# Kernel tuning notes

Measured on AMD Instinct MI355X. Metric: run time of the kernel, lower is better.

Reference implementation:

```python
import jax, jax.numpy as jnp
import numpy as np

N = 12288
E = N * 32  # avg degree 32


def spmm(row, col, w, support):
    # out[i] = sum_{e: row[e]==i} w[e] * support[col[e]]
    return jax.ops.segment_sum(w[:, None] * support[col], row, num_segments=N)


def setup_inputs() -> dict:
    key = jax.random.key(0)
    ks = jax.random.split(key, 7)
    x = jax.random.normal(ks[0], (N, 512), dtype=jnp.float32)
    edge_row = jax.random.randint(ks[1], (E,), 0, N, dtype=jnp.int32)
    edge_col = jax.random.randint(ks[2], (E,), 0, N, dtype=jnp.int32)
    # row-normalized-ish positive edge weights
    edge_w = jax.random.uniform(ks[3], (E,), dtype=jnp.float32) / 32.0
    def xavier(k, fan_in, fan_out):
        bound = float(np.sqrt(6.0 / (fan_in + fan_out)))
        return jax.random.uniform(k, (fan_in, fan_out), jnp.float32, -bound, bound)
    W1 = xavier(ks[4], 512, 256)
    W2 = xavier(ks[5], 256, 128)
    W3 = xavier(ks[6], 128, 64)
    return {"x": x, "edge_row": edge_row, "edge_col": edge_col,
            "edge_w": edge_w, "W1": W1, "W2": W2, "W3": W3}


def reference(x, edge_row, edge_col, edge_w, W1, W2, W3):
    # GNNLayer 1 (active=True): tanh(x @ W) then spmm(adj, .)
    z1 = spmm(edge_row, edge_col, edge_w, jnp.tanh(x @ W1))
    # GNNLayer 2 (active=True)
    z2 = spmm(edge_row, edge_col, edge_w, jnp.tanh(z1 @ W2))
    # GNNLayer 3 (active=False): no activation
    z_igae = spmm(edge_row, edge_col, edge_w, z2 @ W3)  # [N, 64]
    # reconstructed adjacency: sigmoid(z z^T), [N, N]
    z_igae_adj = jax.nn.sigmoid(z_igae @ z_igae.T)
    return (z_igae, z_igae_adj)
```

## Files before the change

kernel.cpp:

```cpp
#include <hip/hip_runtime.h>
#include <hip/hip_bf16.h>

#define NNODES 12288
#define NEDGES (NNODES * 32)
#define ELLCAP 128

typedef __attribute__((ext_vector_type(4))) float f32x4;
typedef __attribute__((ext_vector_type(8))) __bf16 bf16x8;

__global__ __launch_bounds__(256) void prep_kernel(const float* __restrict__ W1,
                                                   const float* __restrict__ W2,
                                                   const float* __restrict__ W3,
                                                   __bf16* __restrict__ W1t,
                                                   __bf16* __restrict__ W2t,
                                                   __bf16* __restrict__ W3t,
                                                   int* __restrict__ deg) {
    int i = blockIdx.x * 256 + threadIdx.x;
    if (i < NNODES) { deg[i] = 0; return; }
    int j = i - NNODES;
    if (j < 512 * 256) { W1t[(size_t)(j % 256) * 512 + j / 256] = (__bf16)W1[j]; return; }
    j -= 512 * 256;
    if (j < 256 * 128) { W2t[(size_t)(j % 128) * 256 + j / 128] = (__bf16)W2[j]; return; }
    j -= 256 * 128;
    if (j < 128 * 64) { W3t[(size_t)(j % 64) * 128 + j / 64] = (__bf16)W3[j]; return; }
}

__global__ __launch_bounds__(256) void gemm1_scatter(const float* __restrict__ x,
                                                     const __bf16* __restrict__ W1t,
                                                     __bf16* __restrict__ h1,
                                                     const int* __restrict__ erow,
                                                     const int* __restrict__ ecol,
                                                     const float* __restrict__ ew,
                                                     int* __restrict__ deg,
                                                     int2* __restrict__ ell) {
    if (blockIdx.x >= 384) {
        int e = (blockIdx.x - 384) * 256 + threadIdx.x;
        int r = erow[e];
        int p = atomicAdd(&deg[r], 1);
        int2 cw; cw.x = ecol[e]; cw.y = __float_as_int(ew[e]);
        ell[(size_t)r * ELLCAP + p] = cw;
        return;
    }
    constexpr int K = 512, Nc = 256;
    int wave = threadIdx.x >> 6, lane = threadIdx.x & 63;
    int lr = lane & 15, kg = lane >> 4;
    int m0 = (blockIdx.x % 96) * 128 + wave * 32;
    int n0 = (blockIdx.x / 96) * 64;
    f32x4 acc[2][4];
#pragma unroll
    for (int mi = 0; mi < 2; mi++)
#pragma unroll
        for (int ni = 0; ni < 4; ni++) acc[mi][ni] = (f32x4){0.f, 0.f, 0.f, 0.f};
#pragma unroll
    for (int k0 = 0; k0 < K; k0 += 32) {
        bf16x8 af[2], bf[4];
#pragma unroll
        for (int mi = 0; mi < 2; mi++) {
            const float* ap = x + (size_t)(m0 + mi * 16 + lr) * K + k0 + kg * 8;
            f32x4 a0 = *(const f32x4*)ap;
            f32x4 a1 = *(const f32x4*)(ap + 4);
#pragma unroll
            for (int j = 0; j < 4; j++) { af[mi][j] = (__bf16)a0[j]; af[mi][4 + j] = (__bf16)a1[j]; }
        }
#pragma unroll
        for (int ni = 0; ni < 4; ni++)
            bf[ni] = *(const bf16x8*)(W1t + (size_t)(n0 + ni * 16 + lr) * K + k0 + kg * 8);
#pragma unroll
        for (int mi = 0; mi < 2; mi++)
#pragma unroll
            for (int ni = 0; ni < 4; ni++)
                acc[mi][ni] = __builtin_amdgcn_mfma_f32_16x16x32_bf16(af[mi], bf[ni], acc[mi][ni], 0, 0, 0);
    }
#pragma unroll
    for (int mi = 0; mi < 2; mi++)
#pragma unroll
        for (int ni = 0; ni < 4; ni++) {
            int col = n0 + ni * 16 + lr;
            int rowb = m0 + mi * 16 + kg * 4;
#pragma unroll
            for (int r = 0; r < 4; r++)
                h1[(size_t)(rowb + r) * Nc + col] = (__bf16)tanhf(acc[mi][ni][r]);
        }
}

template <int K, int NOUT, bool TANH>
__global__ __launch_bounds__(16 * K / 8) void fused_spmm_gemm(const int* __restrict__ deg,
                                                              const int2* __restrict__ ell,
                                                              const __bf16* __restrict__ h_in,
                                                              const __bf16* __restrict__ Wt,
                                                              __bf16* __restrict__ h_out) {
    constexpr int L = K / 8;
    __shared__ __bf16 zs[16][K + 4];
    int tid = threadIdx.x;
    int rloc = tid / L;
    int f8 = (tid % L) * 8;
    int rglob = blockIdx.x * 16 + rloc;
    int d = deg[rglob];
    const int2* er = ell + (size_t)rglob * ELLCAP;
    float acc[8] = {};
#pragma unroll 8
    for (int e = 0; e < d; e++) {
        int2 cw = er[e];
        float w = __int_as_float(cw.y);
        bf16x8 hv = *(const bf16x8*)(h_in + (size_t)cw.x * K + f8);
#pragma unroll
        for (int j = 0; j < 8; j++) acc[j] = fmaf(w, (float)hv[j], acc[j]);
    }
    bf16x8 o;
#pragma unroll
    for (int j = 0; j < 8; j++) o[j] = (__bf16)acc[j];
    *(bf16x8*)&zs[rloc][f8] = o;
    __syncthreads();
    int wave = tid >> 6, lane = tid & 63;
    int lr = lane & 15, kg = lane >> 4;
    f32x4 c = (f32x4){0.f, 0.f, 0.f, 0.f};
#pragma unroll
    for (int ks = 0; ks < K / 32; ks++) {
        bf16x8 a = *(const bf16x8*)&zs[lr][ks * 32 + kg * 8];
        bf16x8 b = *(const bf16x8*)(Wt + (size_t)(wave * 16 + lr) * K + ks * 32 + kg * 8);
        c = __builtin_amdgcn_mfma_f32_16x16x32_bf16(a, b, c, 0, 0, 0);
    }
#pragma unroll
    for (int r = 0; r < 4; r++) {
        float v = c[r];
        if (TANH) v = tanhf(v);
        h_out[(size_t)(blockIdx.x * 16 + kg * 4 + r) * NOUT + wave * 16 + lr] = (__bf16)v;
    }
}

__global__ __launch_bounds__(256) void spmm_final(const int* __restrict__ deg,
                                                  const int2* __restrict__ ell,
                                                  const __bf16* __restrict__ h,
                                                  __bf16* __restrict__ z,
                                                  float* __restrict__ zf) {
    int r = blockIdx.x * 32 + threadIdx.x / 8;
    int f8 = (threadIdx.x & 7) * 8;
    int d = deg[r];
    const int2* er = ell + (size_t)r * ELLCAP;
    float acc[8] = {};
#pragma unroll 8
    for (int e = 0; e < d; e++) {
        int2 cw = er[e];
        float w = __int_as_float(cw.y);
        bf16x8 hv = *(const bf16x8*)(h + (size_t)cw.x * 64 + f8);
#pragma unroll
        for (int j = 0; j < 8; j++) acc[j] = fmaf(w, (float)hv[j], acc[j]);
    }
    bf16x8 o;
#pragma unroll
    for (int j = 0; j < 8; j++) o[j] = (__bf16)acc[j];
    *(bf16x8*)(z + (size_t)r * 64 + f8) = o;
    f32x4 o0, o1;
#pragma unroll
    for (int j = 0; j < 4; j++) { o0[j] = acc[j]; o1[j] = acc[4 + j]; }
    *(f32x4*)(zf + (size_t)r * 64 + f8) = o0;
    *(f32x4*)(zf + (size_t)r * 64 + f8 + 4) = o1;
}

__global__ __launch_bounds__(256) void zzt_sigmoid(const __bf16* __restrict__ Z,
                                                   float* __restrict__ out) {
    __shared__ float tile[2][16][260];
    int wave = threadIdx.x >> 6;
    int lane = threadIdx.x & 63;
    int lr = lane & 15;
    int kg = lane >> 4;
    int r0 = blockIdx.y * 64;
    int c0blk = blockIdx.x * 256;
    int c0 = c0blk + wave * 64;
    bf16x8 af[4][2], bfr[4][2];
#pragma unroll
    for (int i = 0; i < 4; i++)
#pragma unroll
        for (int ks = 0; ks < 2; ks++) {
            af[i][ks]  = *(const bf16x8*)(Z + (size_t)(r0 + i * 16 + lr) * 64 + ks * 32 + kg * 8);
            bfr[i][ks] = *(const bf16x8*)(Z + (size_t)(c0 + i * 16 + lr) * 64 + ks * 32 + kg * 8);
        }
    f32x4 acc[4][4];
#pragma unroll
    for (int mi = 0; mi < 4; mi++)
#pragma unroll
        for (int ni = 0; ni < 4; ni++) acc[mi][ni] = (f32x4){0.f, 0.f, 0.f, 0.f};
#pragma unroll
    for (int mi = 0; mi < 4; mi++)
#pragma unroll
        for (int ni = 0; ni < 4; ni++) {
            acc[mi][ni] = __builtin_amdgcn_mfma_f32_16x16x32_bf16(af[mi][0], bfr[ni][0], acc[mi][ni], 0, 0, 0);
            acc[mi][ni] = __builtin_amdgcn_mfma_f32_16x16x32_bf16(af[mi][1], bfr[ni][1], acc[mi][ni], 0, 0, 0);
        }
#pragma unroll
    for (int ni = 0; ni < 4; ni++) {
        int colb = wave * 64 + ni * 16 + lr;
#pragma unroll
        for (int r = 0; r < 4; r++) {
            float e = __expf(-acc[0][ni][r]);
            tile[0][kg * 4 + r][colb] = __builtin_amdgcn_rcpf(1.f + e);
        }
    }
    __syncthreads();
#pragma unroll
    for (int p = 0; p < 4; p++) {
        if (p < 3) {
#pragma unroll
            for (int ni = 0; ni < 4; ni++) {
                int colb = wave * 64 + ni * 16 + lr;
#pragma unroll
                for (int r = 0; r < 4; r++) {
                    float e = __expf(-acc[p + 1][ni][r]);
                    tile[(p + 1) & 1][kg * 4 + r][colb] = __builtin_amdgcn_rcpf(1.f + e);
                }
            }
        }
#pragma unroll
        for (int it = 0; it < 4; it++) {
            int rowl = it * 4 + wave;
            size_t grow = (size_t)(r0 + p * 16 + rowl);
            *(f32x4*)(out + grow * NNODES + c0blk + lane * 4) = *(const f32x4*)&tile[p & 1][rowl][lane * 4];
        }
        __syncthreads();
    }
}

extern "C" void kernel_launch(void* const* d_in, const int* in_sizes, int n_in,
                              void* d_out, int out_size, void* d_ws, size_t ws_size,
                              hipStream_t stream) {
    (void)in_sizes; (void)n_in; (void)out_size; (void)ws_size;
    const float* x  = (const float*)d_in[0];
    const int* erow = (const int*)d_in[1];
    const int* ecol = (const int*)d_in[2];
    const float* ew = (const float*)d_in[3];
    const float* W1 = (const float*)d_in[4];
    const float* W2 = (const float*)d_in[5];
    const float* W3 = (const float*)d_in[6];
    float* z_igae = (float*)d_out;
    float* adj = (float*)d_out + (size_t)NNODES * 64;

    char* ws = (char*)d_ws;
    size_t off = 0;
    auto alloc = [&](size_t bytes) {
        void* p = ws + off;
        off += (bytes + 255) & ~(size_t)255;
        return p;
    };
    __bf16* W1t = (__bf16*)alloc((size_t)512 * 256 * 2);
    __bf16* W2t = (__bf16*)alloc((size_t)256 * 128 * 2);
    __bf16* W3t = (__bf16*)alloc((size_t)128 * 64 * 2);
    __bf16* h1  = (__bf16*)alloc((size_t)NNODES * 256 * 2);
    __bf16* h2  = (__bf16*)alloc((size_t)NNODES * 128 * 2);
    __bf16* h3  = (__bf16*)alloc((size_t)NNODES * 64 * 2);
    __bf16* Zb  = (__bf16*)alloc((size_t)NNODES * 64 * 2);
    int* deg    = (int*)alloc(NNODES * 4);
    int2* ell   = (int2*)alloc((size_t)NNODES * ELLCAP * 8);

    prep_kernel<<<(NNODES + 512 * 256 + 256 * 128 + 128 * 64 + 255) / 256, 256, 0, stream>>>(
        W1, W2, W3, W1t, W2t, W3t, deg);
    gemm1_scatter<<<384 + NEDGES / 256, 256, 0, stream>>>(x, W1t, h1, erow, ecol, ew, deg, ell);
    fused_spmm_gemm<256, 128, true><<<NNODES / 16, 512, 0, stream>>>(deg, ell, h1, W2t, h2);
    fused_spmm_gemm<128, 64, false><<<NNODES / 16, 256, 0, stream>>>(deg, ell, h2, W3t, h3);
    spmm_final<<<NNODES / 32, 256, 0, stream>>>(deg, ell, h3, Zb, z_igae);
    zzt_sigmoid<<<dim3(NNODES / 256, NNODES / 64), 256, 0, stream>>>((const __bf16*)Zb, adj);
}
```

Before: 230.1 us.

## Reorder layer GEMMs before SpMM gathers to shrink gathered feature width

Uses associativity (A·H)·W = A·(H·W) so that each layer's dense GEMM runs before the sparse aggregation. The edge gathers then read 128-wide rows instead of 256 in layer 2, and 64-wide rows instead of 128 in layer 3. The aim is to cut the gather memory traffic that dominates the SpMM kernels. The cost is one extra kernel launch and an extra intermediate buffer. Rounding also changes because bf16 rounding now happens at different points.

```diff
diff --git a/kernel.cpp b/kernel.cpp
--- a/kernel.cpp
+++ b/kernel.cpp
@@ -83,13 +83,55 @@
         }
 }
 
-template <int K, int NOUT, bool TANH>
-__global__ __launch_bounds__(16 * K / 8) void fused_spmm_gemm(const int* __restrict__ deg,
-                                                              const int2* __restrict__ ell,
-                                                              const __bf16* __restrict__ h_in,
-                                                              const __bf16* __restrict__ Wt,
-                                                              __bf16* __restrict__ h_out) {
-    constexpr int L = K / 8;
+template <bool TANH, int K>
+__global__ __launch_bounds__(256) void gemm_mfma(const __bf16* __restrict__ A,
+                                                 const __bf16* __restrict__ Wt,
+                                                 __bf16* __restrict__ C, int Nc) {
+    int wave = threadIdx.x >> 6, lane = threadIdx.x & 63;
+    int lr = lane & 15, kg = lane >> 4;
+    int m0 = blockIdx.x * 128 + wave * 32;
+    int n0 = blockIdx.y * 64;
+    f32x4 acc[2][4];
+#pragma unroll
+    for (int mi = 0; mi < 2; mi++)
+#pragma unroll
+        for (int ni = 0; ni < 4; ni++) acc[mi][ni] = (f32x4){0.f, 0.f, 0.f, 0.f};
+#pragma unroll
+    for (int k0 = 0; k0 < K; k0 += 32) {
+        bf16x8 af[2], bf[4];
+#pragma unroll
+        for (int mi = 0; mi < 2; mi++)
+            af[mi] = *(const bf16x8*)(A + (size_t)(m0 + mi * 16 + lr) * K + k0 + kg * 8);
+#pragma unroll
+        for (int ni = 0; ni < 4; ni++)
+            bf[ni] = *(const bf16x8*)(Wt + (size_t)(n0 + ni * 16 + lr) * K + k0 + kg * 8);
+#pragma unroll
+        for (int mi = 0; mi < 2; mi++)
+#pragma unroll
+            for (int ni = 0; ni < 4; ni++)
+                acc[mi][ni] = __builtin_amdgcn_mfma_f32_16x16x32_bf16(af[mi], bf[ni], acc[mi][ni], 0, 0, 0);
+    }
+#pragma unroll
+    for (int mi = 0; mi < 2; mi++)
+#pragma unroll
+        for (int ni = 0; ni < 4; ni++) {
+            int col = n0 + ni * 16 + lr;
+            int rowb = m0 + mi * 16 + kg * 4;
+#pragma unroll
+            for (int r = 0; r < 4; r++) {
+                float v = acc[mi][ni][r];
+                if (TANH) v = tanhf(v);
+                C[(size_t)(rowb + r) * Nc + col] = (__bf16)v;
+            }
+        }
+}
+
+__global__ __launch_bounds__(256) void fused_spmm_tanh_gemm(const int* __restrict__ deg,
+                                                            const int2* __restrict__ ell,
+                                                            const __bf16* __restrict__ g1,
+                                                            const __bf16* __restrict__ W3t,
+                                                            __bf16* __restrict__ g2) {
+    constexpr int K = 128, NOUT = 64, L = K / 8;
     __shared__ __bf16 zs[16][K + 4];
     int tid = threadIdx.x;
     int rloc = tid / L;
@@ -102,13 +144,13 @@
     for (int e = 0; e < d; e++) {
         int2 cw = er[e];
         float w = __int_as_float(cw.y);
-        bf16x8 hv = *(const bf16x8*)(h_in + (size_t)cw.x * K + f8);
+        bf16x8 hv = *(const bf16x8*)(g1 + (size_t)cw.x * K + f8);
 #pragma unroll
         for (int j = 0; j < 8; j++) acc[j] = fmaf(w, (float)hv[j], acc[j]);
     }
     bf16x8 o;
 #pragma unroll
-    for (int j = 0; j < 8; j++) o[j] = (__bf16)acc[j];
+    for (int j = 0; j < 8; j++) o[j] = (__bf16)tanhf(acc[j]);
     *(bf16x8*)&zs[rloc][f8] = o;
     __syncthreads();
     int wave = tid >> 6, lane = tid & 63;
@@ -117,15 +159,35 @@
 #pragma unroll
     for (int ks = 0; ks < K / 32; ks++) {
         bf16x8 a = *(const bf16x8*)&zs[lr][ks * 32 + kg * 8];
-        bf16x8 b = *(const bf16x8*)(Wt + (size_t)(wave * 16 + lr) * K + ks * 32 + kg * 8);
+        bf16x8 b = *(const bf16x8*)(W3t + (size_t)(wave * 16 + lr) * K + ks * 32 + kg * 8);
         c = __builtin_amdgcn_mfma_f32_16x16x32_bf16(a, b, c, 0, 0, 0);
     }
 #pragma unroll
-    for (int r = 0; r < 4; r++) {
-        float v = c[r];
-        if (TANH) v = tanhf(v);
-        h_out[(size_t)(blockIdx.x * 16 + kg * 4 + r) * NOUT + wave * 16 + lr] = (__bf16)v;
-    }
+    for (int r = 0; r < 4; r++)
+        g2[(size_t)(blockIdx.x * 16 + kg * 4 + r) * NOUT + wave * 16 + lr] = (__bf16)c[r];
+}
+
+__global__ __launch_bounds__(256) void spmm64(const int* __restrict__ deg,
+                                              const int2* __restrict__ ell,
+                                              const __bf16* __restrict__ h,
+                                              __bf16* __restrict__ z) {
+    int r = blockIdx.x * 32 + threadIdx.x / 8;
+    int f8 = (threadIdx.x & 7) * 8;
+    int d = deg[r];
+    const int2* er = ell + (size_t)r * ELLCAP;
+    float acc[8] = {};
+#pragma unroll 8
+    for (int e = 0; e < d; e++) {
+        int2 cw = er[e];
+        float w = __int_as_float(cw.y);
+        bf16x8 hv = *(const bf16x8*)(h + (size_t)cw.x * 64 + f8);
+#pragma unroll
+        for (int j = 0; j < 8; j++) acc[j] = fmaf(w, (float)hv[j], acc[j]);
+    }
+    bf16x8 o;
+#pragma unroll
+    for (int j = 0; j < 8; j++) o[j] = (__bf16)acc[j];
+    *(bf16x8*)(z + (size_t)r * 64 + f8) = o;
 }
 
 __global__ __launch_bounds__(256) void spmm_final(const int* __restrict__ deg,
@@ -245,8 +307,9 @@
     __bf16* W2t = (__bf16*)alloc((size_t)256 * 128 * 2);
     __bf16* W3t = (__bf16*)alloc((size_t)128 * 64 * 2);
     __bf16* h1  = (__bf16*)alloc((size_t)NNODES * 256 * 2);
-    __bf16* h2  = (__bf16*)alloc((size_t)NNODES * 128 * 2);
-    __bf16* h3  = (__bf16*)alloc((size_t)NNODES * 64 * 2);
+    __bf16* g1  = (__bf16*)alloc((size_t)NNODES * 128 * 2);
+    __bf16* g2  = (__bf16*)alloc((size_t)NNODES * 64 * 2);
+    __bf16* t   = (__bf16*)alloc((size_t)NNODES * 64 * 2);
     __bf16* Zb  = (__bf16*)alloc((size_t)NNODES * 64 * 2);
     int* deg    = (int*)alloc(NNODES * 4);
     int2* ell   = (int2*)alloc((size_t)NNODES * ELLCAP * 8);
@@ -254,8 +317,9 @@
     prep_kernel<<<(NNODES + 512 * 256 + 256 * 128 + 128 * 64 + 255) / 256, 256, 0, stream>>>(
         W1, W2, W3, W1t, W2t, W3t, deg);
     gemm1_scatter<<<384 + NEDGES / 256, 256, 0, stream>>>(x, W1t, h1, erow, ecol, ew, deg, ell);
-    fused_spmm_gemm<256, 128, true><<<NNODES / 16, 512, 0, stream>>>(deg, ell, h1, W2t, h2);
-    fused_spmm_gemm<128, 64, false><<<NNODES / 16, 256, 0, stream>>>(deg, ell, h2, W3t, h3);
-    spmm_final<<<NNODES / 32, 256, 0, stream>>>(deg, ell, h3, Zb, z_igae);
+    gemm_mfma<false, 256><<<dim3(NNODES / 128, 2), 256, 0, stream>>>(h1, W2t, g1, 128);
+    fused_spmm_tanh_gemm<<<NNODES / 16, 256, 0, stream>>>(deg, ell, g1, W3t, g2);
+    spmm64<<<NNODES / 32, 256, 0, stream>>>(deg, ell, g2, t);
+    spmm_final<<<NNODES / 32, 256, 0, stream>>>(deg, ell, t, Zb, z_igae);
     zzt_sigmoid<<<dim3(NNODES / 256, NNODES / 64), 256, 0, stream>>>((const __bf16*)Zb, adj);
 }
```

New measurement: 215.7 us. -6.3%, faster.
